# Kernel tuning notes

Hardware: AMD Instinct MI355X
Metric: run time of the kernel (lower is better)

The kernel has to match this reference:

```python
import jax, jax.numpy as jnp
import numpy as np

NUM_EMBEDDINGS = 2048
EMBEDDING_DIM = 512
INPUT_DIM = 256  # input_chan**2 = 16**2
COMMITMENT_COST = 0.25
BN_EPS = 1e-5


def setup_inputs() -> dict:
    key = jax.random.key(0)
    ks = jax.random.split(key, 8)
    B, N = 64, 1024
    inputs = jax.random.normal(ks[0], (B, N, INPUT_DIM), dtype=jnp.float32)
    # embedding init: uniform(-1/K, 1/K) as in the torch module
    emb_scale = 1.0 / NUM_EMBEDDINGS
    embedding = jax.random.uniform(ks[1], (NUM_EMBEDDINGS, EMBEDDING_DIM), dtype=jnp.float32,
                                   minval=-emb_scale, maxval=emb_scale)
    # Linear layers use torch convention W[out, in]
    W1 = jax.random.normal(ks[2], (EMBEDDING_DIM, INPUT_DIM), dtype=jnp.float32) / np.sqrt(INPUT_DIM)
    b1 = jnp.zeros((EMBEDDING_DIM,), dtype=jnp.float32)
    W2 = jax.random.normal(ks[3], (INPUT_DIM, EMBEDDING_DIM), dtype=jnp.float32) / np.sqrt(EMBEDDING_DIM)
    b2 = jnp.zeros((INPUT_DIM,), dtype=jnp.float32)
    # BatchNorm affine params initialized to 1/0 as in the module
    bn1_gamma = jnp.ones((INPUT_DIM,), dtype=jnp.float32)
    bn1_beta = jnp.zeros((INPUT_DIM,), dtype=jnp.float32)
    bn2_gamma = jnp.ones((EMBEDDING_DIM,), dtype=jnp.float32)
    bn2_beta = jnp.zeros((EMBEDDING_DIM,), dtype=jnp.float32)
    return {"inputs": inputs, "bn1_gamma": bn1_gamma, "bn1_beta": bn1_beta,
            "W1": W1, "b1": b1, "embedding": embedding,
            "bn2_gamma": bn2_gamma, "bn2_beta": bn2_beta, "W2": W2, "b2": b2}


def reference(inputs, bn1_gamma, bn1_beta, W1, b1, embedding, bn2_gamma, bn2_beta, W2, b2):
    sg = jax.lax.stop_gradient
    input_shape = inputs.shape
    flat = inputs.reshape(-1, INPUT_DIM)  # [T, D_in]
    # BatchNorm1d in eval mode (running_mean=0, running_var=1); Dropout is identity in eval.
    bn1_scale = 1.0 / jnp.sqrt(1.0 + BN_EPS)
    x = flat * (bn1_gamma * bn1_scale) + bn1_beta
    x = x @ W1.T + b1  # [T, E]
    # pairwise squared distances to codebook, argmin
    distances = (jnp.sum(x * x, axis=1, keepdims=True)
                 + jnp.sum(embedding * embedding, axis=1)
                 - 2.0 * x @ embedding.T)  # [T, K]
    encoding_indices = jnp.argmin(distances, axis=1)  # [T]
    # gather == one-hot @ embedding (same math, same gradient scatter-add)
    quantized = jnp.take(embedding, encoding_indices, axis=0)  # [T, E]
    bn2_scale = 1.0 / jnp.sqrt(1.0 + BN_EPS)
    quantized = quantized * (bn2_gamma * bn2_scale) + bn2_beta
    quantized = (quantized @ W2.T + b2).reshape(input_shape)
    e_latent_loss = jnp.mean((sg(quantized) - inputs) ** 2)
    q_latent_loss = jnp.mean((quantized - sg(inputs)) ** 2)
    loss = q_latent_loss + COMMITMENT_COST * e_latent_loss
    quantized_st = inputs + sg(quantized - inputs)  # straight-through
    T = flat.shape[0]
    usage = jnp.zeros((NUM_EMBEDDINGS,), dtype=jnp.float32).at[encoding_indices].add(1.0) / T
    return (loss, quantized_st, usage)
```

## Files before the change

### kernel.cpp

```cpp
#include <hip/hip_runtime.h>
#include <math.h>
#include <stdint.h>

#define TOK 65536
#define DIN 256
#define EDIM 512
#define KCB 2048
#define NTB 128

#define OFF_MP   0u
#define OFF_CP   524288u
#define OFF_Q    526336u
#define OFF_W2T  1050624u
#define OFF_U    1181696u
#define OFF_CQ   1182208u
#define OFF_BH   1182464u
#define TOT_F    1444608u

typedef short short8 __attribute__((ext_vector_type(8)));
typedef float f32x4 __attribute__((ext_vector_type(4)));

__device__ __forceinline__ unsigned short bf16rne(float x) {
    uint32_t u = __float_as_uint(x);
    u += 0x7fffu + ((u >> 16) & 1u);
    return (unsigned short)(u >> 16);
}
__device__ __forceinline__ void async_load16(const void* g, void* l) {
    __builtin_amdgcn_global_load_lds((const __attribute__((address_space(1))) void*)g,
                                     (__attribute__((address_space(3))) void*)l, 16, 0, 0);
}

__global__ void prep1_kernel(const float* __restrict__ W1, const float* __restrict__ W2,
                             const float* __restrict__ bn1_beta, const float* __restrict__ bn2_gamma,
                             const float* __restrict__ bn2_beta, const float* __restrict__ b2,
                             float* __restrict__ W2T, float* __restrict__ u, float* __restrict__ cQ,
                             float* __restrict__ out) {
    __shared__ float red[256];
    const int b = blockIdx.x, t = threadIdx.x;
    const int gid = b * 256 + t;
    if (gid == 0) out[0] = 0.0f;
    if (gid < KCB) out[1 + TOK * DIN + gid] = 0.0f;
    const float s = 1.0f / sqrtf(1.0f + 1e-5f);
    if (b < EDIM) {
        int e = b;
        W2T[e * DIN + t] = bn2_gamma[e] * s * W2[t * EDIM + e];
        float v = bn1_beta[t] * W1[e * DIN + t];
        red[t] = v; __syncthreads();
        for (int off = 128; off; off >>= 1) { if (t < off) red[t] += red[t + off]; __syncthreads(); }
        if (t == 0) u[e] = red[0];
    } else {
        int o = b - EDIM;
        float v = bn2_beta[t] * W2[o * EDIM + t] + bn2_beta[t + 256] * W2[o * EDIM + t + 256];
        red[t] = v; __syncthreads();
        for (int off = 128; off; off >>= 1) { if (t < off) red[t] += red[t + off]; __syncthreads(); }
        if (t == 0) cQ[o] = b2[o] + red[0];
    }
}

__global__ __launch_bounds__(512) void prep2_kernel(const float* __restrict__ E, const float* __restrict__ W1,
                                                    const float* __restrict__ W2T, const float* __restrict__ bn1_gamma,
                                                    const float* __restrict__ cQ, const float* __restrict__ b1,
                                                    const float* __restrict__ u,
                                                    float* __restrict__ Q, float* __restrict__ cp,
                                                    unsigned short* __restrict__ Bh) {
    __shared__ __align__(16) unsigned short hs[8][264];
    const int t = threadIdx.x;
    const int col = t & 255;
    const int half = __builtin_amdgcn_readfirstlane(t >> 8);
    const int k0 = blockIdx.x * 8;
    const float* __restrict__ Ek = E + ((size_t)k0 + (size_t)half * 4) * EDIM;

    float m[4] = {0, 0, 0, 0};
    float q[4] = {0, 0, 0, 0};
    for (int e0 = 0; e0 < EDIM; e0 += 8) {
        float w1v[8], w2v[8];
#pragma unroll
        for (int j = 0; j < 8; j++) {
            w1v[j] = W1[(e0 + j) * DIN + col];
            w2v[j] = W2T[(e0 + j) * DIN + col];
        }
#pragma unroll
        for (int r = 0; r < 4; r++) {
#pragma unroll
            for (int j = 0; j < 8; j++) {
                float ev = Ek[(size_t)r * EDIM + e0 + j];
                m[r] += ev * w1v[j];
                q[r] += ev * w2v[j];
            }
        }
    }
    const float s = 1.0f / sqrtf(1.0f + 1e-5f);
    const float gs = bn1_gamma[col] * s;
    const float cq = cQ[col];
#pragma unroll
    for (int r = 0; r < 4; r++) {
        Q[(size_t)(k0 + half * 4 + r) * DIN + col] = q[r] + cq;
        hs[half * 4 + r][col] = bf16rne(gs * m[r]);
    }

    {
        const int wv = t >> 6, l = t & 63;
        const float* __restrict__ Er = E + (size_t)(k0 + wv) * EDIM;
        float sa = 0.0f, sb = 0.0f;
#pragma unroll
        for (int i = 0; i < 8; i++) {
            int e = l + i * 64;
            float ev = Er[e];
            float be = b1[e] + u[e];
            sa += ev * be; sb += ev * ev;
        }
        float v = sa - 0.5f * sb;
#pragma unroll
        for (int off = 32; off; off >>= 1) v += __shfl_down(v, off, 64);
        if (l == 0) cp[k0 + wv] = v;
    }

    __syncthreads();

    if (t < 256) {
        const int rr = t & 7, qr = (t >> 3) & 3, kc = t >> 5;
        const int nt = k0 >> 4;
        const int l2 = (k0 & 8) + rr + (qr << 4);
        short8 vh = *(const short8*)&hs[rr][kc * 32 + qr * 8];
        *(short8*)&Bh[((size_t)kc * NTB + nt) * 512 + (size_t)l2 * 8] = vh;
    }
}

__global__ __launch_bounds__(256, 2) void score_fused_kernel(const float* __restrict__ flat,
                                                             const unsigned short* __restrict__ Bh,
                                                             const float* __restrict__ cp,
                                                             const float* __restrict__ Q,
                                                             float* __restrict__ out) {
    __shared__ __align__(16) unsigned short Blds[2][32 * 512];
    __shared__ float mv[2][128];
    __shared__ int   mi[2][128];
    const int t = threadIdx.x, lane = t & 63, w = t >> 6;
    const int wr = w >> 1, wc = w & 1;
    const int m0 = blockIdx.x * 128;
    const int fr = lane & 15, qr = lane >> 4;

    short8 af[8][4];
#pragma unroll
    for (int kc = 0; kc < 8; kc++)
#pragma unroll
        for (int mt = 0; mt < 4; mt++) {
            int row = m0 + wr * 64 + mt * 16 + fr;
            const float* p = flat + (size_t)row * DIN + kc * 32 + qr * 8;
            float4 a = *(const float4*)p;
            float4 b = *(const float4*)(p + 4);
            float f[8] = {a.x, a.y, a.z, a.w, b.x, b.y, b.z, b.w};
            unsigned short* hp = (unsigned short*)&af[kc][mt];
#pragma unroll
            for (int j = 0; j < 8; j++) hp[j] = bf16rne(f[j]);
        }

#pragma unroll
    for (int i = 0; i < 8; i++) {
        int tl = i * 4 + w;
        int kc = tl >> 2, nt = tl & 3;
        async_load16(Bh + ((size_t)kc * NTB + nt) * 512 + lane * 8,
                     &Blds[0][tl * 512 + lane * 8]);
    }
    __syncthreads();

    float bestv[4][4];
    int besti[4][4];
#pragma unroll
    for (int mt = 0; mt < 4; mt++)
#pragma unroll
        for (int r = 0; r < 4; r++) { bestv[mt][r] = -3.4e38f; besti[mt][r] = 0; }

    const f32x4 ZERO4 = {0.f, 0.f, 0.f, 0.f};

#pragma unroll 1
    for (int s = 0; s < 32; s++) {
        const int cur = s & 1;
        if (s < 31) {
            const int nxt = cur ^ 1;
#pragma unroll
            for (int i = 0; i < 8; i++) {
                int tl = i * 4 + w;
                int kc = tl >> 2, nt = tl & 3;
                async_load16(Bh + ((size_t)kc * NTB + (s + 1) * 4 + nt) * 512 + lane * 8,
                             &Blds[nxt][tl * 512 + lane * 8]);
            }
        }
        f32x4 acc[4][2];
        {
            short8 bf0 = *(const short8*)&Blds[cur][(0 * 4 + wc * 2 + 0) * 512 + lane * 8];
            short8 bf1 = *(const short8*)&Blds[cur][(0 * 4 + wc * 2 + 1) * 512 + lane * 8];
#pragma unroll
            for (int mt = 0; mt < 4; mt++) {
                acc[mt][0] = __builtin_amdgcn_mfma_f32_16x16x32_bf16(af[0][mt], bf0, ZERO4, 0, 0, 0);
                acc[mt][1] = __builtin_amdgcn_mfma_f32_16x16x32_bf16(af[0][mt], bf1, ZERO4, 0, 0, 0);
            }
        }
#pragma unroll
        for (int kc = 1; kc < 8; kc++) {
            short8 bf0 = *(const short8*)&Blds[cur][(kc * 4 + wc * 2 + 0) * 512 + lane * 8];
            short8 bf1 = *(const short8*)&Blds[cur][(kc * 4 + wc * 2 + 1) * 512 + lane * 8];
#pragma unroll
            for (int mt = 0; mt < 4; mt++) {
                acc[mt][0] = __builtin_amdgcn_mfma_f32_16x16x32_bf16(af[kc][mt], bf0, acc[mt][0], 0, 0, 0);
                acc[mt][1] = __builtin_amdgcn_mfma_f32_16x16x32_bf16(af[kc][mt], bf1, acc[mt][1], 0, 0, 0);
            }
        }
        const int base = s * 64 + wc * 32 + fr;
        const float cpv0 = cp[base];
        const float cpv1 = cp[base + 16];
#pragma unroll
        for (int mt = 0; mt < 4; mt++)
#pragma unroll
            for (int r = 0; r < 4; r++) {
                float v0 = acc[mt][0][r] + cpv0;
                float v1 = acc[mt][1][r] + cpv1;
                float v = v0; int ci = base;
                if (v1 > v0) { v = v1; ci = base + 16; }
                if (v > bestv[mt][r]) { bestv[mt][r] = v; besti[mt][r] = ci; }
            }
        __syncthreads();
    }

#pragma unroll
    for (int mt = 0; mt < 4; mt++)
#pragma unroll
        for (int r = 0; r < 4; r++) {
            float bv = bestv[mt][r];
            int bc = besti[mt][r];
#pragma unroll
            for (int xm = 1; xm < 16; xm <<= 1) {
                float ov = __shfl_xor(bv, xm, 64);
                int oc = __shfl_xor(bc, xm, 64);
                if (ov > bv || (ov == bv && oc < bc)) { bv = ov; bc = oc; }
            }
            if (fr == 0) {
                int rl = wr * 64 + mt * 16 + qr * 4 + r;
                mv[wc][rl] = bv;
                mi[wc][rl] = bc;
            }
        }
    __syncthreads();

    float lsum = 0.0f;
    for (int rr = 0; rr < 32; rr++) {
        int rl = w * 32 + rr;
        int row = m0 + rl;
        float v0 = mv[0][rl], v1 = mv[1][rl];
        int c0 = mi[0][rl], c1 = mi[1][rl];
        int k = (v1 > v0 || (v1 == v0 && c1 < c0)) ? c1 : c0;
        const float* qr_ = Q + (size_t)k * DIN;
        const float* xr = flat + (size_t)row * DIN;
        float* ob = out + 1 + (size_t)row * DIN;
#pragma unroll
        for (int cc = 0; cc < 4; cc++) {
            int j = lane + 64 * cc;
            float q = qr_[j];
            float d = q - xr[j];
            lsum += d * d;
            ob[j] = q;
        }
        if (lane == 0) atomicAdd(out + 1 + TOK * DIN + k, 1.0f / (float)TOK);
    }
#pragma unroll
    for (int off = 32; off; off >>= 1) lsum += __shfl_down(lsum, off, 64);
    if (lane == 0) atomicAdd(out, lsum * (1.25f / (float)((size_t)TOK * DIN)));
}

extern "C" void kernel_launch(void* const* d_in, const int* in_sizes, int n_in,
                              void* d_out, int out_size, void* d_ws, size_t ws_size,
                              hipStream_t stream) {
    const float* inputs = (const float*)d_in[0];
    const float* bn1_gamma = (const float*)d_in[1];
    const float* bn1_beta  = (const float*)d_in[2];
    const float* W1 = (const float*)d_in[3];
    const float* b1 = (const float*)d_in[4];
    const float* E  = (const float*)d_in[5];
    const float* bn2_gamma = (const float*)d_in[6];
    const float* bn2_beta  = (const float*)d_in[7];
    const float* W2 = (const float*)d_in[8];
    const float* b2 = (const float*)d_in[9];

    float* ws = (float*)d_ws;
    float* cp  = ws + OFF_CP;
    float* Q   = ws + OFF_Q;
    float* W2T = ws + OFF_W2T;
    float* u   = ws + OFF_U;
    float* cQ  = ws + OFF_CQ;
    unsigned short* Bh = (unsigned short*)(ws + OFF_BH);
    float* out = (float*)d_out;

    hipLaunchKernelGGL(prep1_kernel, dim3(768), dim3(256), 0, stream,
                       W1, W2, bn1_beta, bn2_gamma, bn2_beta, b2, W2T, u, cQ, out);
    hipLaunchKernelGGL(prep2_kernel, dim3(256), dim3(512), 0, stream,
                       E, W1, W2T, bn1_gamma, cQ, b1, u, Q, cp, Bh);
    hipLaunchKernelGGL(score_fused_kernel, dim3(512), dim3(256), 0, stream,
                       inputs, Bh, cp, Q, out);
}
```

Measured before the change: 274.7 us.

## Load codebook fragments directly from global into registers, dropping LDS staging

The score kernel no longer stages codebook tiles in double-buffered LDS through async global-to-LDS loads with per-step barriers. Each wave instead reads its own half of the codebook (1024 codes) straight from global memory into registers, prefetching the next tile's fragments between MFMA groups. This removes the shared-memory traffic and the block-wide barriers, at the cost of more global/L2 loads per wave, since waves no longer share one LDS copy, and exposed load latency inside the loop. Candidate indices now come out in ascending order within each lane.

```diff
diff --git a/kernel.cpp b/kernel.cpp
--- a/kernel.cpp
+++ b/kernel.cpp
@@ -24,10 +24,6 @@
     uint32_t u = __float_as_uint(x);
     u += 0x7fffu + ((u >> 16) & 1u);
     return (unsigned short)(u >> 16);
-}
-__device__ __forceinline__ void async_load16(const void* g, void* l) {
-    __builtin_amdgcn_global_load_lds((const __attribute__((address_space(1))) void*)g,
-                                     (__attribute__((address_space(3))) void*)l, 16, 0, 0);
 }
 
 __global__ void prep1_kernel(const float* __restrict__ W1, const float* __restrict__ W2,
@@ -131,7 +127,6 @@
                                                              const float* __restrict__ cp,
                                                              const float* __restrict__ Q,
                                                              float* __restrict__ out) {
-    __shared__ __align__(16) unsigned short Blds[2][32 * 512];
     __shared__ float mv[2][128];
     __shared__ int   mi[2][128];
     const int t = threadIdx.x, lane = t & 63, w = t >> 6;
@@ -154,14 +149,7 @@
             for (int j = 0; j < 8; j++) hp[j] = bf16rne(f[j]);
         }
 
-#pragma unroll
-    for (int i = 0; i < 8; i++) {
-        int tl = i * 4 + w;
-        int kc = tl >> 2, nt = tl & 3;
-        async_load16(Bh + ((size_t)kc * NTB + nt) * 512 + lane * 8,
-                     &Blds[0][tl * 512 + lane * 8]);
-    }
-    __syncthreads();
+    const unsigned short* __restrict__ Bhaving = Bh + ((size_t)(wc * 64)) * 512 + (size_t)lane * 8;
 
     float bestv[4][4];
     int besti[4][4];
@@ -172,53 +160,49 @@
 
     const f32x4 ZERO4 = {0.f, 0.f, 0.f, 0.f};
 
+    short8 bf[8];
+#pragma unroll
+    for (int kc = 0; kc < 8; kc++)
+        bf[kc] = *(const short8*)(Bhaving + ((size_t)kc * NTB) * 512);
+
 #pragma unroll 1
-    for (int s = 0; s < 32; s++) {
-        const int cur = s & 1;
-        if (s < 31) {
-            const int nxt = cur ^ 1;
-#pragma unroll
-            for (int i = 0; i < 8; i++) {
-                int tl = i * 4 + w;
-                int kc = tl >> 2, nt = tl & 3;
-                async_load16(Bh + ((size_t)kc * NTB + (s + 1) * 4 + nt) * 512 + lane * 8,
-                             &Blds[nxt][tl * 512 + lane * 8]);
-            }
-        }
-        f32x4 acc[4][2];
-        {
-            short8 bf0 = *(const short8*)&Blds[cur][(0 * 4 + wc * 2 + 0) * 512 + lane * 8];
-            short8 bf1 = *(const short8*)&Blds[cur][(0 * 4 + wc * 2 + 1) * 512 + lane * 8];
-#pragma unroll
-            for (int mt = 0; mt < 4; mt++) {
-                acc[mt][0] = __builtin_amdgcn_mfma_f32_16x16x32_bf16(af[0][mt], bf0, ZERO4, 0, 0, 0);
-                acc[mt][1] = __builtin_amdgcn_mfma_f32_16x16x32_bf16(af[0][mt], bf1, ZERO4, 0, 0, 0);
-            }
-        }
-#pragma unroll
-        for (int kc = 1; kc < 8; kc++) {
-            short8 bf0 = *(const short8*)&Blds[cur][(kc * 4 + wc * 2 + 0) * 512 + lane * 8];
-            short8 bf1 = *(const short8*)&Blds[cur][(kc * 4 + wc * 2 + 1) * 512 + lane * 8];
-#pragma unroll
-            for (int mt = 0; mt < 4; mt++) {
-                acc[mt][0] = __builtin_amdgcn_mfma_f32_16x16x32_bf16(af[kc][mt], bf0, acc[mt][0], 0, 0, 0);
-                acc[mt][1] = __builtin_amdgcn_mfma_f32_16x16x32_bf16(af[kc][mt], bf1, acc[mt][1], 0, 0, 0);
-            }
-        }
-        const int base = s * 64 + wc * 32 + fr;
-        const float cpv0 = cp[base];
-        const float cpv1 = cp[base + 16];
+    for (int nt = 0; nt < 64; nt++) {
+        f32x4 acc[4];
+        acc[0] = __builtin_amdgcn_mfma_f32_16x16x32_bf16(af[0][0], bf[0], ZERO4, 0, 0, 0);
+        acc[1] = __builtin_amdgcn_mfma_f32_16x16x32_bf16(af[0][1], bf[0], ZERO4, 0, 0, 0);
+        acc[2] = __builtin_amdgcn_mfma_f32_16x16x32_bf16(af[0][2], bf[0], ZERO4, 0, 0, 0);
+        acc[3] = __builtin_amdgcn_mfma_f32_16x16x32_bf16(af[0][3], bf[0], ZERO4, 0, 0, 0);
+#pragma unroll
+        for (int kc = 1; kc < 4; kc++) {
+#pragma unroll
+            for (int mt = 0; mt < 4; mt++)
+                acc[mt] = __builtin_amdgcn_mfma_f32_16x16x32_bf16(af[kc][mt], bf[kc], acc[mt], 0, 0, 0);
+        }
+        if (nt < 63) {
+#pragma unroll
+            for (int kc = 0; kc < 4; kc++)
+                bf[kc] = *(const short8*)(Bhaving + ((size_t)kc * NTB + nt + 1) * 512);
+        }
+#pragma unroll
+        for (int kc = 4; kc < 8; kc++) {
+#pragma unroll
+            for (int mt = 0; mt < 4; mt++)
+                acc[mt] = __builtin_amdgcn_mfma_f32_16x16x32_bf16(af[kc][mt], bf[kc], acc[mt], 0, 0, 0);
+        }
+        if (nt < 63) {
+#pragma unroll
+            for (int kc = 4; kc < 8; kc++)
+                bf[kc] = *(const short8*)(Bhaving + ((size_t)kc * NTB + nt + 1) * 512);
+        }
+        const int base = wc * 1024 + nt * 16 + fr;
+        const float cpv = cp[base];
 #pragma unroll
         for (int mt = 0; mt < 4; mt++)
 #pragma unroll
             for (int r = 0; r < 4; r++) {
-                float v0 = acc[mt][0][r] + cpv0;
-                float v1 = acc[mt][1][r] + cpv1;
-                float v = v0; int ci = base;
-                if (v1 > v0) { v = v1; ci = base + 16; }
-                if (v > bestv[mt][r]) { bestv[mt][r] = v; besti[mt][r] = ci; }
-            }
-        __syncthreads();
+                float v = acc[mt][r] + cpv;
+                if (v > bestv[mt][r]) { bestv[mt][r] = v; besti[mt][r] = base; }
+            }
     }
 
 #pragma unroll
```

Measured after the change: 272.7 us. Within noise of the previous version (-0.8%).
